# Optimization experiments

Measured on AMD Instinct MI355X. Metric: run time of the kernel, lower is better.

## Reference

```python
import jax, jax.numpy as jnp
import numpy as np
import math

NUM_HEADS = 16
SPARSITY_RATIO = 0.1
MASK_KEY_SEED = 42


def _sparse_mask(seq_length):
    """Band (+/-2 around diagonal) OR random num_random columns per row. [S,S] float32 of {0,1}."""
    i = jnp.arange(seq_length)
    band = (jnp.abs(i[:, None] - i[None, :]) <= 2).astype(jnp.float32)
    num_random = max(1, int(seq_length * SPARSITY_RATIO))
    u = jax.random.uniform(jax.random.key(MASK_KEY_SEED), (seq_length, seq_length))
    _, idx = jax.lax.top_k(u, num_random)  # [S, num_random] random distinct cols per row
    rand_mask = jnp.zeros((seq_length, seq_length), jnp.float32).at[i[:, None], idx].set(1.0)
    return jnp.maximum(band, rand_mask)


def setup_inputs() -> dict:
    key = jax.random.key(0)
    ks = jax.random.split(key, 7)
    B, S, H = 2, 2048, 1024
    scale = 0.02
    return {
        "hidden_states": jax.random.normal(ks[0], (B, S, H), jnp.float32),
        "Wq": jax.random.normal(ks[1], (H, H), jnp.float32) * scale,
        "bq": jnp.zeros((H,), jnp.float32),
        "Wk": jax.random.normal(ks[2], (H, H), jnp.float32) * scale,
        "bk": jnp.zeros((H,), jnp.float32),
        "Wv": jax.random.normal(ks[3], (H, H), jnp.float32) * scale,
        "bv": jnp.zeros((H,), jnp.float32),
    }


def reference(hidden_states, Wq, bq, Wk, bk, Wv, bv):
    B, S, H = hidden_states.shape
    nh = NUM_HEADS
    hd = H // nh

    def proj(W, b):
        # nn.Linear: x @ W.T + b, then [B,S,nh,hd] -> [B,nh,S,hd]
        y = jnp.einsum('bsh,oh->bso', hidden_states, W) + b
        return y.reshape(B, S, nh, hd).transpose(0, 2, 1, 3)

    q = proj(Wq, bq)
    k = proj(Wk, bk)
    v = proj(Wv, bv)

    scores = jnp.einsum('bhqd,bhkd->bhqk', q, k) / math.sqrt(hd)
    mask = _sparse_mask(S)  # [S,S], broadcast over batch and heads
    scores = scores * mask  # multiplicative mask (masked scores become 0, NOT -inf)
    probs = jax.nn.softmax(scores, axis=-1)
    ctx = jnp.einsum('bhqk,bhkd->bhqd', probs, v)
    return ctx.transpose(0, 2, 1, 3).reshape(B, S, H)
```

## Files before the change

kernel.cpp:

```cpp
#include <hip/hip_runtime.h>


typedef unsigned int u32;
typedef unsigned short u16;
typedef float f32x4 __attribute__((ext_vector_type(4)));
typedef short s16x8 __attribute__((ext_vector_type(8)));
typedef u16  u16x8 __attribute__((ext_vector_type(8)));
typedef u32  u32x4 __attribute__((ext_vector_type(4)));
typedef u16  u16x4 __attribute__((ext_vector_type(4)));

__device__ __forceinline__ u16 f2bf(float f) {
  u32 u = __builtin_bit_cast(u32, f);
  return (u16)((u + 0x7FFFu + ((u >> 16) & 1u)) >> 16);
}

__device__ __forceinline__ void async16(void* lds, const void* g) {
  __builtin_amdgcn_global_load_lds((const __attribute__((address_space(1))) u32*)g,
                                   (__attribute__((address_space(3))) u32*)lds, 16, 0, 0);
}

__global__ __launch_bounds__(256) void cast_kernel(const float* __restrict__ src,
                                                   u16* __restrict__ dst, int n4) {
  int i = blockIdx.x * 256 + threadIdx.x;
  if (i < n4) {
    float4 v = ((const float4*)src)[i];
    u16x4 o = { f2bf(v.x), f2bf(v.y), f2bf(v.z), f2bf(v.w) };
    ((u16x4*)dst)[i] = o;
  }
}

__device__ __forceinline__ void threefry(u32 x0, u32 x1, u32& y0, u32& y1) {
  const u32 k0 = 0u, k1 = 42u, k2 = 0u ^ 42u ^ 0x1BD11BDAu;
  x0 += k0; x1 += k1;
#define TFR(r) { x0 += x1; x1 = (x1 << r) | (x1 >> (32 - r)); x1 ^= x0; }
  TFR(13) TFR(15) TFR(26) TFR(6)  x0 += k1; x1 += k2 + 1u;
  TFR(17) TFR(29) TFR(16) TFR(24) x0 += k2; x1 += k0 + 2u;
  TFR(13) TFR(15) TFR(26) TFR(6)  x0 += k0; x1 += k1 + 3u;
  TFR(17) TFR(29) TFR(16) TFR(24) x0 += k1; x1 += k2 + 4u;
  TFR(13) TFR(15) TFR(26) TFR(6)  x0 += k2; x1 += k0 + 5u;
#undef TFR
  y0 = x0; y1 = x1;
}

#define NRAND 204

__global__ __launch_bounds__(256) void mask_kernel(u32* __restrict__ maskbits) {
  __shared__ u32 hist[256];
  __shared__ u32 mwords[64];
  __shared__ u32 candV[128];
  __shared__ u32 candC[128];
  __shared__ u32 used[128];
  __shared__ u32 scal[4];

  const int tid = threadIdx.x;
  const int row = blockIdx.x;
  hist[tid] = 0;
  if (tid < 64) mwords[tid] = 0;
  if (tid < 128) used[tid] = 0;
  if (tid == 0) scal[2] = 0;
  __syncthreads();

  u32 k23[8];
#pragma unroll
  for (int j = 0; j < 8; ++j) {
    u32 c = (u32)tid * 8u + (u32)j;
    u32 flat = (u32)row * 2048u + c;
    u32 y0, y1; threefry(0u, flat, y0, y1);
    u32 bits = y0 ^ y1;
    k23[j] = bits >> 9;
    atomicAdd(&hist[k23[j] >> 15], 1u);
  }
  __syncthreads();
  for (int off = 1; off < 256; off <<= 1) {
    u32 add = (tid + off < 256) ? hist[tid + off] : 0u;
    __syncthreads();
    hist[tid] += add;
    __syncthreads();
  }
  u32 Sv = hist[tid];
  u32 Sn = (tid < 255) ? hist[tid + 1] : 0u;
  if (Sv >= NRAND && Sn < NRAND) { scal[0] = (u32)tid; scal[1] = NRAND - Sn; }
  __syncthreads();
  const u32 bin = scal[0];
  const u32 need = scal[1];
#pragma unroll
  for (int j = 0; j < 8; ++j) {
    if ((k23[j] >> 15) == bin) {
      u32 p = atomicAdd(&scal[2], 1u);
      if (p < 128u) { candV[p] = k23[j]; candC[p] = (u32)tid * 8u + (u32)j; }
    }
  }
  __syncthreads();
  if (tid == 0) {
    int n = (int)(scal[2] < 128u ? scal[2] : 128u);
    for (u32 t = 0; t < need; ++t) {
      int best = -1;
      for (int i2 = 0; i2 < n; ++i2) {
        if (used[i2]) continue;
        if (best < 0 || candV[i2] > candV[best] ||
            (candV[i2] == candV[best] && candC[i2] < candC[best])) best = i2;
      }
      if (best < 0) break;
      used[best] = 1;
      atomicOr(&mwords[candC[best] >> 5], 1u << (candC[best] & 31u));
    }
  }
#pragma unroll
  for (int j = 0; j < 8; ++j) {
    u32 c = (u32)tid * 8u + (u32)j;
    if ((k23[j] >> 15) > bin) atomicOr(&mwords[c >> 5], 1u << (c & 31u));
  }
  if (tid < 5) {
    int c = row - 2 + tid;
    if (c >= 0 && c < 2048) atomicOr(&mwords[c >> 5], 1u << (c & 31u));
  }
  __syncthreads();
  if (tid < 64) maskbits[row * 64 + tid] = mwords[tid];
}

__global__ __launch_bounds__(256) void gemm_qkv(
    const u16* __restrict__ Xbf, const u16* __restrict__ Wbf3,
    const float* __restrict__ bq, const float* __restrict__ bk,
    const float* __restrict__ bv,
    u16* __restrict__ Qbf, u16* __restrict__ Kbf, u16* __restrict__ VtB) {
  __shared__ u16 smem[128 * 136];
  u16* As = smem;
  u16* Bs = smem + 4096;

  const int tid  = threadIdx.x;
  const int lane = tid & 63;
  const int w    = tid >> 6;
  const int wr = w >> 1, wc = w & 1;
  const int l15 = lane & 15, l4 = lane >> 4;
  const int mBase = blockIdx.x * 128;
  const int nBase = blockIdx.y * 128;
  const int z = blockIdx.z;
  const u16* Bmat = Wbf3 + z * 1048576;
  const float* bias = (z == 0) ? bq : (z == 1) ? bk : bv;

  const int ci1 = tid, ci2 = tid + 256;
  const int r1 = ci1 >> 2, c1 = ci1 & 3, cc1 = c1 ^ ((r1 >> 1) & 3);
  const int r2 = ci2 >> 2, c2 = ci2 & 3, cc2 = c2 ^ ((r2 >> 1) & 3);

  f32x4 acc[4][4];
#pragma unroll
  for (int i = 0; i < 4; ++i)
#pragma unroll
    for (int j = 0; j < 4; ++j) acc[i][j] = {0.f, 0.f, 0.f, 0.f};

  for (int k0 = 0; k0 < 1024; k0 += 32) {
    async16(As + ci1 * 8, Xbf + (mBase + r1) * 1024 + k0 + cc1 * 8);
    async16(As + ci2 * 8, Xbf + (mBase + r2) * 1024 + k0 + cc2 * 8);
    async16(Bs + ci1 * 8, Bmat + (nBase + r1) * 1024 + k0 + cc1 * 8);
    async16(Bs + ci2 * 8, Bmat + (nBase + r2) * 1024 + k0 + cc2 * 8);
    __syncthreads();
    s16x8 a[4], b[4];
#pragma unroll
    for (int f = 0; f < 4; ++f) {
      int rl = wr * 64 + f * 16 + l15;
      a[f] = *(const s16x8*)(As + rl * 32 + ((l4 ^ ((rl >> 1) & 3)) * 8));
    }
#pragma unroll
    for (int f = 0; f < 4; ++f) {
      int rl = wc * 64 + f * 16 + l15;
      b[f] = *(const s16x8*)(Bs + rl * 32 + ((l4 ^ ((rl >> 1) & 3)) * 8));
    }
#pragma unroll
    for (int i = 0; i < 4; ++i)
#pragma unroll
      for (int j = 0; j < 4; ++j)
        acc[i][j] = __builtin_amdgcn_mfma_f32_16x16x32_bf16(a[i], b[j], acc[i][j], 0, 0, 0);
    __syncthreads();
  }

  const float scale = (z == 0) ? 0.125f : 1.0f;
  if (z < 2) {
    u16* dst = (z == 0) ? Qbf : Kbf;
#pragma unroll
    for (int i = 0; i < 4; ++i)
#pragma unroll
      for (int j = 0; j < 4; ++j) {
        int ng = nBase + wc * 64 + j * 16 + l15;
        int h = ng >> 6, d = ng & 63;
        float bb = bias[ng];
#pragma unroll
        for (int r = 0; r < 4; ++r) {
          int mg = mBase + wr * 64 + i * 16 + l4 * 4 + r;
          int bbi = mg >> 11, s = mg & 2047;
          dst[(((bbi * 16 + h) * 2048 + s) * 64) + d] = f2bf((acc[i][j][r] + bb) * scale);
        }
      }
  } else {
    u16* ct = smem;
#pragma unroll
    for (int i = 0; i < 4; ++i)
#pragma unroll
      for (int j = 0; j < 4; ++j) {
        int nl = wc * 64 + j * 16 + l15;
        float bb = bias[nBase + nl];
        int base = nl * 136 + wr * 64 + 16 * l4 + i;
#pragma unroll
        for (int r = 0; r < 4; ++r)
          ct[base + 4 * r] = f2bf(acc[i][j][r] + bb);
      }
    __syncthreads();
#pragma unroll
    for (int it = 0; it < 8; ++it) {
      int ci = tid + it * 256;
      int nl = ci >> 4, m8 = ci & 15;
      int ng = nBase + nl, mg = mBase + m8 * 8;
      int h = ng >> 6, d = ng & 63;
      int bbi = mg >> 11, s = mg & 2047;
      s16x8 v = *(const s16x8*)(ct + nl * 136 + m8 * 8);
      *(s16x8*)(VtB + (((bbi * 16 + h) * 64 + d) * 2048) + s) = v;
    }
  }
}

__global__ __launch_bounds__(256, 4) void attn_kernel(
    const u16* __restrict__ Qbf, const u16* __restrict__ Kbf,
    const u16* __restrict__ Vt, const u32* __restrict__ maskbits,
    float* __restrict__ out) {
  __shared__ u16 Kb[2][4096];
  __shared__ u16 Vb[2][4096];
  __shared__ u16 Pls[4][1152];

  const int tid  = threadIdx.x;
  const int lane = tid & 63;
  const int w    = tid >> 6;
  const int l15 = lane & 15, l4 = lane >> 4;

  const int lin = blockIdx.x + 32 * blockIdx.y;
  const int wg  = (lin & 7) * 128 + (lin >> 3);
  const int qt = wg & 31;
  const int bh = wg >> 5;
  const int qbase = qt * 64;

  const int qrow = qbase + w * 16 + l15;
  const u16* qp = Qbf + ((bh * 2048 + qrow) * 64) + l4 * 8;
  s16x8 qa0 = *(const s16x8*)(qp);
  s16x8 qa1 = *(const s16x8*)(qp + 32);

  const u32* mrow[4];
#pragma unroll
  for (int r = 0; r < 4; ++r)
    mrow[r] = maskbits + (qbase + w * 16 + l4 * 4 + r) * 64;

  const f32x4 fzero = {0.f, 0.f, 0.f, 0.f};
  f32x4 acc[4];
#pragma unroll
  for (int d = 0; d < 4; ++d) acc[d] = fzero;
  float rs[4] = {0.f, 0.f, 0.f, 0.f};

  const int rkA = tid >> 3, cA = tid & 7, csA = cA ^ (rkA & 7);
  const int ci2 = tid + 256;
  const int rkB = ci2 >> 3, cB = ci2 & 7, csB = cB ^ (rkB & 7);
  const u16* kgbase = Kbf + (size_t)(bh * 2048) * 64;
  const u16* vgbase = Vt + (size_t)(bh * 64) * 2048;

  async16(Kb[0] + tid * 8, kgbase + rkA * 64 + csA * 8);
  async16(Kb[0] + ci2 * 8, kgbase + rkB * 64 + csB * 8);
  async16(Vb[0] + tid * 8, vgbase + rkA * 2048 + csA * 8);
  async16(Vb[0] + ci2 * 8, vgbase + rkB * 2048 + csB * 8);
  asm volatile("s_waitcnt vmcnt(0)" ::: "memory");
  __syncthreads();

  u16* Pw = Pls[w];

  for (int kt = 0; kt < 32; ++kt) {
    const int kb = kt * 64;
    const int cur = kt & 1;

    uint2 mw2[4];
#pragma unroll
    for (int r = 0; r < 4; ++r)
      mw2[r] = *(const uint2*)(mrow[r] + kt * 2);

    if (kt < 31) {
      const u16* kg = kgbase + (kb + 64) * 64;
      const u16* vg = vgbase + kb + 64;
      async16(Kb[cur ^ 1] + tid * 8, kg + rkA * 64 + csA * 8);
      async16(Kb[cur ^ 1] + ci2 * 8, kg + rkB * 64 + csB * 8);
      async16(Vb[cur ^ 1] + tid * 8, vg + rkA * 2048 + csA * 8);
      async16(Vb[cur ^ 1] + ci2 * 8, vg + rkB * 2048 + csB * 8);
    }

    f32x4 sc[4];
#pragma unroll
    for (int fn = 0; fn < 4; ++fn) {
      int key = fn * 16 + l15;
      s16x8 kf0 = *(const s16x8*)(Kb[cur] + key * 64 + ((l4 ^ (key & 7)) * 8));
      s16x8 kf1 = *(const s16x8*)(Kb[cur] + key * 64 + (((l4 + 4) ^ (key & 7)) * 8));
      sc[fn] = __builtin_amdgcn_mfma_f32_16x16x32_bf16(qa0, kf0, fzero, 0, 0, 0);
      sc[fn] = __builtin_amdgcn_mfma_f32_16x16x32_bf16(qa1, kf1, sc[fn], 0, 0, 0);
    }

#pragma unroll
    for (int r = 0; r < 4; ++r) {
      float p[4];
#pragma unroll
      for (int fn = 0; fn < 4; ++fn) {
        u32 word = (fn < 2) ? mw2[r].x : mw2[r].y;
        u32 bp = (u32)((fn & 1) * 16 + l15);
        float sv = ((word >> bp) & 1u) ? sc[fn][r] : 0.0f;
        p[fn] = __expf(sv);
      }
      rs[r] += (p[0] + p[1]) + (p[2] + p[3]);
      u16x4 pk = { f2bf(p[0]), f2bf(p[1]), f2bf(p[2]), f2bf(p[3]) };
      *(u16x4*)(Pw + (l4 * 4 + r) * 72 + l15 * 4) = pk;
    }

    __builtin_amdgcn_sched_barrier(0);

    u16x8 t0 = *(const u16x8*)(Pw + l15 * 72 + l4 * 8);
    u16x8 t1 = *(const u16x8*)(Pw + l15 * 72 + 32 + l4 * 8);
    s16x8 pa0 = __builtin_bit_cast(s16x8, t0);
    s16x8 pa1 = __builtin_bit_cast(s16x8, t1);
#pragma unroll
    for (int df = 0; df < 4; ++df) {
      int dl = df * 16 + l15;
      s16x8 vf0 = *(const s16x8*)(Vb[cur] + dl * 64 + ((l4 ^ (dl & 7)) * 8));
      s16x8 vf1 = *(const s16x8*)(Vb[cur] + dl * 64 + (((l4 + 4) ^ (dl & 7)) * 8));
      acc[df] = __builtin_amdgcn_mfma_f32_16x16x32_bf16(pa0, vf0, acc[df], 0, 0, 0);
      acc[df] = __builtin_amdgcn_mfma_f32_16x16x32_bf16(pa1, vf1, acc[df], 0, 0, 0);
    }

    asm volatile("s_waitcnt vmcnt(0)" ::: "memory");
    __syncthreads();
  }

#pragma unroll
  for (int r = 0; r < 4; ++r) {
    float v = rs[r];
    v += __shfl_xor(v, 1); v += __shfl_xor(v, 2);
    v += __shfl_xor(v, 4); v += __shfl_xor(v, 8);
    rs[r] = 1.0f / v;
  }
  const int b = bh >> 4, h = bh & 15;
#pragma unroll
  for (int df = 0; df < 4; ++df) {
    int col = h * 64 + df * 16 + l15;
#pragma unroll
    for (int r = 0; r < 4; ++r) {
      int qg = qbase + w * 16 + l4 * 4 + r;
      out[(b * 2048 + qg) * 1024 + col] = acc[df][r] * rs[r];
    }
  }
}

extern "C" void kernel_launch(void* const* d_in, const int* in_sizes, int n_in,
                              void* d_out, int out_size, void* d_ws, size_t ws_size,
                              hipStream_t stream) {
  const float* hs = (const float*)d_in[0];
  const float* Wq = (const float*)d_in[1];
  const float* bq = (const float*)d_in[2];
  const float* Wk = (const float*)d_in[3];
  const float* bk = (const float*)d_in[4];
  const float* Wv = (const float*)d_in[5];
  const float* bv = (const float*)d_in[6];
  float* out = (float*)d_out;
  char* ws = (char*)d_ws;

  u32* maskbits = (u32*)(ws);
  u16* Xbf  = (u16*)(ws + 524288);
  u16* Wbf3 = (u16*)(ws + 524288 + 8388608);
  u16* Qbf  = (u16*)(ws + 15204352);
  u16* Kbf  = (u16*)(ws + 23592960);
  u16* Vt   = (u16*)(ws + 31981568);

  cast_kernel<<<4096, 256, 0, stream>>>(hs, Xbf, 1048576);
  cast_kernel<<<1024, 256, 0, stream>>>(Wq, Wbf3,           262144);
  cast_kernel<<<1024, 256, 0, stream>>>(Wk, Wbf3 + 1048576, 262144);
  cast_kernel<<<1024, 256, 0, stream>>>(Wv, Wbf3 + 2097152, 262144);
  mask_kernel<<<2048, 256, 0, stream>>>(maskbits);
  gemm_qkv<<<dim3(32, 8, 3), 256, 0, stream>>>(Xbf, Wbf3, bq, bk, bv, Qbf, Kbf, Vt);
  attn_kernel<<<dim3(32, 32), 256, 0, stream>>>(Qbf, Kbf, Vt, maskbits, out);
}
```

Measured before the change: 250.9 us.

## Merge cast launches, swizzle GEMM block order, truncate P to bf16

The four fp32-to-bf16 cast launches become one kernel that picks its source by block index, which removes launch overhead. The QKV GEMM remaps its block indices so that consecutive blocks are spread across XCDs in a chunked order, aiming for better L2 reuse. The attention kernel now packs the softmax probabilities into bf16 by truncating with bit masks instead of round-to-nearest, which saves ALU work in the inner loop. The truncation adds a small bias to the numerics.

```diff
diff --git a/kernel.cpp b/kernel.cpp
--- a/kernel.cpp
+++ b/kernel.cpp
@@ -5,7 +5,6 @@
 typedef unsigned short u16;
 typedef float f32x4 __attribute__((ext_vector_type(4)));
 typedef short s16x8 __attribute__((ext_vector_type(8)));
-typedef u16  u16x8 __attribute__((ext_vector_type(8)));
 typedef u32  u32x4 __attribute__((ext_vector_type(4)));
 typedef u16  u16x4 __attribute__((ext_vector_type(4)));
 
@@ -19,14 +18,21 @@
                                    (__attribute__((address_space(3))) u32*)lds, 16, 0, 0);
 }
 
-__global__ __launch_bounds__(256) void cast_kernel(const float* __restrict__ src,
-                                                   u16* __restrict__ dst, int n4) {
-  int i = blockIdx.x * 256 + threadIdx.x;
-  if (i < n4) {
-    float4 v = ((const float4*)src)[i];
-    u16x4 o = { f2bf(v.x), f2bf(v.y), f2bf(v.z), f2bf(v.w) };
-    ((u16x4*)dst)[i] = o;
-  }
+__global__ __launch_bounds__(256) void cast_all(
+    const float* __restrict__ hs, const float* __restrict__ Wq,
+    const float* __restrict__ Wk, const float* __restrict__ Wv,
+    u16* __restrict__ Xbf, u16* __restrict__ Wbf3) {
+  const int b = blockIdx.x;
+  const float* src;
+  u16* dst;
+  int i;
+  if (b < 4096)      { src = hs; dst = Xbf;            i = b * 256 + threadIdx.x; }
+  else if (b < 5120) { src = Wq; dst = Wbf3;           i = (b - 4096) * 256 + threadIdx.x; }
+  else if (b < 6144) { src = Wk; dst = Wbf3 + 1048576; i = (b - 5120) * 256 + threadIdx.x; }
+  else               { src = Wv; dst = Wbf3 + 2097152; i = (b - 6144) * 256 + threadIdx.x; }
+  float4 v = ((const float4*)src)[i];
+  u16x4 o = { f2bf(v.x), f2bf(v.y), f2bf(v.z), f2bf(v.w) };
+  ((u16x4*)dst)[i] = o;
 }
 
 __device__ __forceinline__ void threefry(u32 x0, u32 x1, u32& y0, u32& y1) {
@@ -132,9 +138,12 @@
   const int w    = tid >> 6;
   const int wr = w >> 1, wc = w & 1;
   const int l15 = lane & 15, l4 = lane >> 4;
-  const int mBase = blockIdx.x * 128;
-  const int nBase = blockIdx.y * 128;
-  const int z = blockIdx.z;
+
+  const int lin = blockIdx.x + 32 * (blockIdx.y + 8 * blockIdx.z);
+  const int wg  = (lin & 7) * 96 + (lin >> 3);
+  const int bx = wg & 31, by = (wg >> 5) & 7, z = wg >> 8;
+  const int mBase = bx * 128;
+  const int nBase = by * 128;
   const u16* Bmat = Wbf3 + z * 1048576;
   const float* bias = (z == 0) ? bq : (z == 1) ? bk : bv;
 
@@ -223,7 +232,7 @@
     float* __restrict__ out) {
   __shared__ u16 Kb[2][4096];
   __shared__ u16 Vb[2][4096];
-  __shared__ u16 Pls[4][1152];
+  __shared__ __align__(16) u32 Pls[4][576];
 
   const int tid  = threadIdx.x;
   const int lane = tid & 63;
@@ -265,7 +274,7 @@
   asm volatile("s_waitcnt vmcnt(0)" ::: "memory");
   __syncthreads();
 
-  u16* Pw = Pls[w];
+  u32* Pw = Pls[w];
 
   for (int kt = 0; kt < 32; ++kt) {
     const int kb = kt * 64;
@@ -306,14 +315,19 @@
         p[fn] = __expf(sv);
       }
       rs[r] += (p[0] + p[1]) + (p[2] + p[3]);
-      u16x4 pk = { f2bf(p[0]), f2bf(p[1]), f2bf(p[2]), f2bf(p[3]) };
-      *(u16x4*)(Pw + (l4 * 4 + r) * 72 + l15 * 4) = pk;
+      u32 b0 = __builtin_bit_cast(u32, p[0]);
+      u32 b1 = __builtin_bit_cast(u32, p[1]);
+      u32 b2 = __builtin_bit_cast(u32, p[2]);
+      u32 b3 = __builtin_bit_cast(u32, p[3]);
+      u32* wp = Pw + (l4 * 4 + r) * 36 + l15 * 2;
+      wp[0] = (b0 >> 16) | (b1 & 0xffff0000u);
+      wp[1] = (b2 >> 16) | (b3 & 0xffff0000u);
     }
 
     __builtin_amdgcn_sched_barrier(0);
 
-    u16x8 t0 = *(const u16x8*)(Pw + l15 * 72 + l4 * 8);
-    u16x8 t1 = *(const u16x8*)(Pw + l15 * 72 + 32 + l4 * 8);
+    u32x4 t0 = *(const u32x4*)(Pw + l15 * 36 + l4 * 4);
+    u32x4 t1 = *(const u32x4*)(Pw + l15 * 36 + 16 + l4 * 4);
     s16x8 pa0 = __builtin_bit_cast(s16x8, t0);
     s16x8 pa1 = __builtin_bit_cast(s16x8, t1);
 #pragma unroll
@@ -368,10 +382,7 @@
   u16* Kbf  = (u16*)(ws + 23592960);
   u16* Vt   = (u16*)(ws + 31981568);
 
-  cast_kernel<<<4096, 256, 0, stream>>>(hs, Xbf, 1048576);
-  cast_kernel<<<1024, 256, 0, stream>>>(Wq, Wbf3,           262144);
-  cast_kernel<<<1024, 256, 0, stream>>>(Wk, Wbf3 + 1048576, 262144);
-  cast_kernel<<<1024, 256, 0, stream>>>(Wv, Wbf3 + 2097152, 262144);
+  cast_all<<<7168, 256, 0, stream>>>(hs, Wq, Wk, Wv, Xbf, Wbf3);
   mask_kernel<<<2048, 256, 0, stream>>>(maskbits);
   gemm_qkv<<<dim3(32, 8, 3), 256, 0, stream>>>(Xbf, Wbf3, bq, bk, bv, Qbf, Kbf, Vt);
   attn_kernel<<<dim3(32, 32), 256, 0, stream>>>(Qbf, Kbf, Vt, maskbits, out);
```

Result: no change. 250.9 us (-0.0%).
